# Optimization experiments

Hardware: AMD Instinct MI355X
Metric: run time of the kernel (lower is better)

## Reference

```python
import jax, jax.numpy as jnp
import numpy as np

B, S, IN, E, H, NL = 64, 512, 1024, 128, 8, 4
D = E // H  # head dim = 16


def setup_inputs() -> dict:
    key = jax.random.key(0)
    ks = jax.random.split(key, 12)
    rn = lambda k, shape: jax.random.normal(k, shape, jnp.float32) * 0.02
    x = jax.random.normal(ks[0], (B, S, IN), jnp.float32)
    # per-recording valid lengths; recording 0 full-length so no attention key row is all-masked
    lengths = jax.random.randint(ks[1], (B,), 1, S + 1).at[0].set(S)
    key_padding_mask = jnp.arange(S)[None, :] >= lengths[:, None]  # (B,S) True = pad
    return {
        'x': x,
        'key_padding_mask': key_padding_mask,
        'embed_w': rn(ks[2], (IN, E)), 'embed_b': jnp.zeros((E,), jnp.float32),
        'qkv_w': rn(ks[3], (NL, 3, E, E)), 'qkv_b': jnp.zeros((NL, 3, E), jnp.float32),
        'out_w': rn(ks[4], (NL, E, E)), 'out_b': jnp.zeros((NL, E), jnp.float32),
        'ln_g': jnp.ones((NL, E), jnp.float32), 'ln_b': jnp.zeros((NL, E), jnp.float32),
        'ff1_w': rn(ks[5], (NL, E, 4 * E)), 'ff1_b': jnp.zeros((NL, 4 * E), jnp.float32),
        'ff2_w': rn(ks[6], (NL, 4 * E, E)), 'ff2_b': jnp.zeros((NL, E), jnp.float32),
        'fc1_w': rn(ks[7], (E, 32)), 'fc1_b': jnp.zeros((32,), jnp.float32),
        'fc2_w': rn(ks[8], (32, 1)), 'fc2_b': jnp.zeros((1,), jnp.float32),
    }


def _ln(x, g, b):
    m = x.mean(-1, keepdims=True)
    v = x.var(-1, keepdims=True)
    return (x - m) / jnp.sqrt(v + 1e-5) * g + b


def _pos_enc(s, e):
    pos = jnp.arange(s, dtype=jnp.float32)[:, None]
    i = jnp.arange(e)[None, :]
    angle = pos / jnp.power(jnp.float32(10000.0), (2 * (i // 2)).astype(jnp.float32) / e)
    return jnp.where(i % 2 == 0, jnp.sin(angle), jnp.cos(angle))  # (S,E)


def reference(x, key_padding_mask, embed_w, embed_b, qkv_w, qkv_b, out_w, out_b,
              ln_g, ln_b, ff1_w, ff1_b, ff2_w, ff2_b, fc1_w, fc1_b, fc2_w, fc2_b):
    h = x @ embed_w + embed_b  # (B,S,E)
    pe = _pos_enc(S, E)
    scale = 1.0 / jnp.sqrt(jnp.float32(D))
    # module uses batch_first=False MHA on (B,S,E): attention runs across recordings.
    # key_padding_mask.T -> (S,B): masked keys are recordings, per epoch position.
    keymask = key_padding_mask.T[:, None, None, :]  # (S,1,1,B)
    for l in range(NL):
        h = h + pe[None]  # pos enc re-added every block (as in source)
        res = h
        q = (h @ qkv_w[l, 0] + qkv_b[l, 0]).reshape(B, S, H, D)
        k = (h @ qkv_w[l, 1] + qkv_b[l, 1]).reshape(B, S, H, D)
        v = (h @ qkv_w[l, 2] + qkv_b[l, 2]).reshape(B, S, H, D)
        scores = jnp.einsum('ishd,jshd->shij', q, k) * scale  # (S,H,B,B)
        scores = jnp.where(keymask, -jnp.inf, scores)
        attn = jax.nn.softmax(scores, axis=-1)
        o = jnp.einsum('shij,jshd->ishd', attn, v).reshape(B, S, E)
        o = o @ out_w[l] + out_b[l]
        h = _ln(o + res, ln_g[l], ln_b[l])
        res = h
        ffo = jax.nn.relu(h @ ff1_w[l] + ff1_b[l]) @ ff2_w[l] + ff2_b[l]
        h = _ln(ffo + res, ln_g[l], ln_b[l])  # same LN params reused, as in source
    # masked mean pool over epochs (vectorized replacement of the python loop)
    valid = (~key_padding_mask).astype(h.dtype)  # (B,S)
    mean = jnp.einsum('bse,bs->be', h, valid) / valid.sum(axis=1)[:, None]
    out = jax.nn.relu(mean @ fc1_w + fc1_b) @ fc2_w + fc2_b  # (B,1)
    return jax.nn.sigmoid(out)
```

## Files before the change

kernel.cpp:

```cpp
#include <hip/hip_runtime.h>

#define Bb 64
#define Ss 512
#define INn 1024
#define Ee 128
#define Hh 8
#define Dd 16
#define NLl 4

typedef unsigned short u16;
typedef __attribute__((ext_vector_type(8))) short short8;
typedef __attribute__((ext_vector_type(4))) float f32x4;

__device__ __forceinline__ float b2f(unsigned u) { return __uint_as_float(u << 16); }
__device__ __forceinline__ u16 f2b(float f) {
    unsigned u = __float_as_uint(f);
    unsigned r = u + 0x7FFFu + ((u >> 16) & 1u);
    return (u16)(r >> 16);
}
__device__ __forceinline__ uint2 pk4(float4 f) {
    uint2 r;
    r.x = (unsigned)f2b(f.x) | ((unsigned)f2b(f.y) << 16);
    r.y = (unsigned)f2b(f.z) | ((unsigned)f2b(f.w) << 16);
    return r;
}

#define GLOAD_LDS16(g, l) __builtin_amdgcn_global_load_lds( \
    (const __attribute__((address_space(1))) void*)(g),     \
    (__attribute__((address_space(3))) void*)(l), 16, 0, 0)

#define MFMA16(a, b, c) __builtin_amdgcn_mfma_f32_16x16x32_bf16((a), (b), (c), 0, 0, 0)

__global__ __launch_bounds__(256) void prep_kernel(const unsigned char* __restrict__ m,
                                                   int* __restrict__ lengths,
                                                   float* __restrict__ pe,
                                                   const float* __restrict__ ew,
                                                   const float* __restrict__ qw,
                                                   const float* __restrict__ ow,
                                                   const float* __restrict__ f1w,
                                                   const float* __restrict__ f2w,
                                                   u16* __restrict__ we, u16* __restrict__ wq,
                                                   u16* __restrict__ wo, u16* __restrict__ wf1,
                                                   u16* __restrict__ wf2) {
    const int bid = blockIdx.x, tid = threadIdx.x;
    if (bid == 0) {
        __shared__ int lf[3];
        __shared__ int part[256];
        if (tid < 3) lf[tid] = 0;
        __syncthreads();
        int l0 = 0, l1 = 0, l23 = 0;
        for (int i = tid * 128; i < tid * 128 + 128; ++i) {
            if (m[i]) { int md = i & 3; if (md == 0) l0 = 1; else if (md == 1) l1 = 1; else l23 = 1; }
        }
        if (l0) atomicOr(&lf[0], 1);
        if (l1) atomicOr(&lf[1], 1);
        if (l23) atomicOr(&lf[2], 1);
        __syncthreads();
        int enc = lf[1] ? 1 : (lf[2] ? 2 : 0);
        int b = tid >> 2, q = tid & 3, cnt = 0;
        for (int s = q * 128; s < q * 128 + 128; ++s) {
            int idx = b * Ss + s;
            int mm;
            if (enc == 1)      mm = (m[idx] != 0);
            else if (enc == 2) mm = (((const float*)(const void*)m)[idx] != 0.0f);
            else               mm = (((const int*)(const void*)m)[idx] != 0);
            cnt += (mm == 0);
        }
        part[tid] = cnt;
        __syncthreads();
        if (tid < 64)
            lengths[tid] = part[tid * 4] + part[tid * 4 + 1] + part[tid * 4 + 2] + part[tid * 4 + 3];
        return;
    }
    if (bid <= 32) {
        for (int i = tid; i < 2048; i += 256) {
            int idx = (bid - 1) * 2048 + i;
            int s = idx >> 7, e = idx & 127;
            float expo = (float)(2 * (e >> 1)) * (1.0f / 128.0f);
            float freq = powf(10000.0f, -expo);
            float angle = (float)s * freq;
            pe[idx] = (e & 1) ? cosf(angle) : sinf(angle);
        }
        return;
    }
    int tb = bid - 33;
    const float* src; u16* dst; int K, N, tile;
    if (tb < 32)       { src = ew;  dst = we;  K = 1024; N = 128; tile = tb; }
    else if (tb < 80)  { int b = tb - 32;  int mat = b >> 2; src = qw  + (size_t)mat * 16384; dst = wq  + (size_t)mat * 16384; K = 128; N = 128; tile = b & 3; }
    else if (tb < 96)  { int b = tb - 80;  int mat = b >> 2; src = ow  + (size_t)mat * 16384; dst = wo  + (size_t)mat * 16384; K = 128; N = 128; tile = b & 3; }
    else if (tb < 160) { int b = tb - 96;  int mat = b >> 4; src = f1w + (size_t)mat * 65536; dst = wf1 + (size_t)mat * 65536; K = 128; N = 512; tile = b & 15; }
    else               { int b = tb - 160; int mat = b >> 4; src = f2w + (size_t)mat * 65536; dst = wf2 + (size_t)mat * 65536; K = 512; N = 128; tile = b & 15; }
    int ktiles = K >> 6;
    int k0 = (tile % ktiles) * 64, n0 = (tile / ktiles) * 64;
    __shared__ __align__(16) u16 t_s[64 * 68];
    int r = tid >> 2, cq = (tid & 3) * 16;
    const float* sp = src + (size_t)(k0 + r) * N + n0 + cq;
#pragma unroll
    for (int i = 0; i < 4; ++i) {
        float4 f = *(const float4*)(sp + 4 * i);
        *(uint2*)&t_s[r * 68 + cq + 4 * i] = pk4(f);
    }
    __syncthreads();
    u16 tmp[16];
#pragma unroll
    for (int kk = 0; kk < 16; ++kk) tmp[kk] = t_s[(cq + kk) * 68 + r];
    int rowg = n0 + r;
    int x = (rowg & 7) << 3;
    u16* base = dst + (size_t)rowg * K;
    *(uint4*)(base + ((k0 + cq) ^ x))     = ((uint4*)tmp)[0];
    *(uint4*)(base + ((k0 + cq + 8) ^ x)) = ((uint4*)tmp)[1];
}

__global__ __launch_bounds__(256) void embed_gemm(const float* __restrict__ X,
                                                  const u16* __restrict__ Wt,
                                                  const float* __restrict__ bias,
                                                  const float* __restrict__ pe,
                                                  u16* __restrict__ C) {
    __shared__ __align__(16) u16 Af[64 * 68];
    __shared__ __align__(16) u16 Bs[2][128 * 64];
    const int tid = threadIdx.x;
    const int w = tid >> 6, lane = tid & 63, l16 = lane & 15, lhi = lane >> 4;
    const int row0 = blockIdx.x * 64;
    const int xr = (l16 & 7) << 3;
    f32x4 acc[8];
#pragma unroll
    for (int ni = 0; ni < 8; ++ni) acc[ni] = (f32x4){0.f, 0.f, 0.f, 0.f};

    const int ar = tid >> 2, ak = (tid & 3) * 16;
    const int crow = tid >> 3, cc8 = (tid & 7) * 8;
    const int wave_lds = w * 512;
    const u16* Bbase = Wt + cc8;
    const float* Arow = X + (size_t)(row0 + ar) * 1024 + ak;

#pragma unroll
    for (int i = 0; i < 4; ++i)
        GLOAD_LDS16(Bbase + (size_t)(i * 32 + crow) * 1024, &Bs[0][i * 2048 + wave_lds]);

    for (int it = 0; it < 16; ++it) {
        const int k0 = it * 64;
        __syncthreads();
#pragma unroll
        for (int i = 0; i < 4; ++i) {
            float4 f = *(const float4*)(Arow + k0 + 4 * i);
            *(uint2*)&Af[ar * 68 + ak + 4 * i] = pk4(f);
        }
        __syncthreads();
        if (it < 15) {
#pragma unroll
            for (int i = 0; i < 4; ++i)
                GLOAD_LDS16(Bbase + (size_t)(i * 32 + crow) * 1024 + k0 + 64,
                            &Bs[(it + 1) & 1][i * 2048 + wave_lds]);
        }
#pragma unroll
        for (int ks = 0; ks < 2; ++ks) {
            short8 af;
            ((uint2*)&af)[0] = *(const uint2*)&Af[(w * 16 + l16) * 68 + ks * 32 + lhi * 8];
            ((uint2*)&af)[1] = *(const uint2*)&Af[(w * 16 + l16) * 68 + ks * 32 + lhi * 8 + 4];
#pragma unroll
            for (int ni = 0; ni < 8; ++ni) {
                short8 bfr = *(const short8*)&Bs[it & 1][(ni * 16 + l16) * 64 + ((ks * 32 + lhi * 8) ^ xr)];
                acc[ni] = MFMA16(af, bfr, acc[ni]);
            }
        }
    }
    float biasr[8];
#pragma unroll
    for (int ni = 0; ni < 8; ++ni) biasr[ni] = bias[ni * 16 + l16];
#pragma unroll
    for (int reg = 0; reg < 4; ++reg) {
        int r = row0 + w * 16 + lhi * 4 + reg;
        int s = r & 511;
        int bidx = r >> 9;
        int orow = s * 64 + bidx;
        int xo = (bidx & 7) << 3;
        const float* per = pe + (size_t)s * 128;
        u16* crw = C + (size_t)orow * 128;
#pragma unroll
        for (int ni = 0; ni < 8; ++ni) {
            int c = ni * 16 + l16;
            crw[c ^ xo] = f2b(acc[ni][reg] + biasr[ni] + per[c]);
        }
    }
}

__global__ __launch_bounds__(256) void qkv_gemm(const u16* __restrict__ A,
                                                const u16* __restrict__ Wt,
                                                const float* __restrict__ bias,
                                                u16* __restrict__ Cq,
                                                u16* __restrict__ Ckv) {
    __shared__ __align__(16) u16 As[128 * 128];
    __shared__ __align__(16) u16 Bs[128 * 128];
    const int tid = threadIdx.x, w = tid >> 6, lane = tid & 63;
    const int l16 = lane & 15, lhi = lane >> 4;
    const int row0 = blockIdx.x * 128, col0 = blockIdx.y * 128;
    const int so = w * 512 + lane * 8;
    const int xr = (l16 & 7) << 3;
#pragma unroll
    for (int i = 0; i < 8; ++i) {
        GLOAD_LDS16(A + (size_t)row0 * 128 + i * 2048 + so, &As[i * 2048 + w * 512]);
        GLOAD_LDS16(Wt + (size_t)col0 * 128 + i * 2048 + so, &Bs[i * 2048 + w * 512]);
    }
    __syncthreads();
    f32x4 acc[2][8];
#pragma unroll
    for (int mi = 0; mi < 2; ++mi)
#pragma unroll
        for (int ni = 0; ni < 8; ++ni) acc[mi][ni] = (f32x4){0.f, 0.f, 0.f, 0.f};
#pragma unroll
    for (int ks = 0; ks < 4; ++ks) {
        const int ko = (ks * 32 + lhi * 8) ^ xr;
        short8 af[2], bfr[8];
#pragma unroll
        for (int mi = 0; mi < 2; ++mi)
            af[mi] = *(const short8*)&As[(w * 32 + mi * 16 + l16) * 128 + ko];
#pragma unroll
        for (int ni = 0; ni < 8; ++ni)
            bfr[ni] = *(const short8*)&Bs[(ni * 16 + l16) * 128 + ko];
#pragma unroll
        for (int mi = 0; mi < 2; ++mi)
#pragma unroll
            for (int ni = 0; ni < 8; ++ni)
                acc[mi][ni] = MFMA16(af[mi], bfr[ni], acc[mi][ni]);
    }
    float biasr[8];
#pragma unroll
    for (int ni = 0; ni < 8; ++ni) biasr[ni] = bias[col0 + ni * 16 + l16];
#pragma unroll
    for (int mi = 0; mi < 2; ++mi)
#pragma unroll
        for (int reg = 0; reg < 4; ++reg) {
            int r = row0 + w * 32 + mi * 16 + lhi * 4 + reg;
            u16* crw; int cbase;
            if (col0 == 0) { crw = Cq + (size_t)r * 128; cbase = 0; }
            else           { crw = Ckv + (size_t)r * 256; cbase = col0 - 128; }
#pragma unroll
            for (int ni = 0; ni < 8; ++ni)
                crw[cbase + ni * 16 + l16] = f2b(acc[mi][ni][reg] + biasr[ni]);
        }
}

__global__ __launch_bounds__(256) void attn_ff_kernel(const u16* __restrict__ qb,
                                                      const u16* __restrict__ kvb,
                                                      const u16* __restrict__ wo,
                                                      const float* __restrict__ outb,
                                                      const u16* __restrict__ w1t,
                                                      const u16* __restrict__ w2t,
                                                      const float* __restrict__ b1,
                                                      const float* __restrict__ b2,
                                                      const int* __restrict__ lengths,
                                                      const float* __restrict__ gamma,
                                                      const float* __restrict__ beta,
                                                      const float* __restrict__ pe,
                                                      u16* __restrict__ h) {
    const int d = blockIdx.x;
    const int s = ((d & 7) << 1) + ((d >> 3) & 1) + ((d >> 4) << 4);
    const int tid = threadIdx.x, w = tid >> 6, lane = tid & 63;
    const int l16 = lane & 15, lhi = lane >> 4;
    const int xr = (l16 & 7) << 3;
    const int so = w * 512 + lane * 8;

    __shared__ __align__(16) u16 arena[39424];
    __shared__ int len_s[64];
    u16* o_s  = arena;
    u16* A_s  = arena + 8704;
    u16* T_s  = arena + 16896;
    u16* Ps   = arena + 20992;
    u16* W1_s = arena + 20992;
    u16* W2_s = arena + 29184;

    if (tid < 64) len_s[tid] = lengths[tid];
    __syncthreads();

    bool mk[4];
#pragma unroll
    for (int jt = 0; jt < 4; ++jt) mk[jt] = (s >= len_s[jt * 16 + l16]);

    u16* pw = Ps + w * 4608;
#pragma unroll
    for (int hp = 0; hp < 2; ++hp) {
        const int hh = w * 2 + hp;
        short8 af[4];
#pragma unroll
        for (int it = 0; it < 4; ++it) {
            af[it] = (short8){0, 0, 0, 0, 0, 0, 0, 0};
            if (lhi < 2)
                af[it] = *(const short8*)(qb + ((size_t)(s * 64 + it * 16 + l16)) * 128 + hh * 16 + lhi * 8);
        }
        f32x4 sf[4][4];
#pragma unroll
        for (int jt = 0; jt < 4; ++jt) {
            short8 bf = (short8){0, 0, 0, 0, 0, 0, 0, 0};
            if (lhi < 2)
                bf = *(const short8*)(kvb + ((size_t)(s * 64 + jt * 16 + l16)) * 256 + hh * 16 + lhi * 8);
#pragma unroll
            for (int it = 0; it < 4; ++it) {
                f32x4 z = {0.f, 0.f, 0.f, 0.f};
                sf[it][jt] = MFMA16(af[it], bf, z);
            }
        }
        float inv[4][4];
#pragma unroll
        for (int it = 0; it < 4; ++it) {
#pragma unroll
            for (int reg = 0; reg < 4; ++reg) {
                float vv[4], mx = -1e30f;
#pragma unroll
                for (int jt = 0; jt < 4; ++jt) {
                    float xv = mk[jt] ? -1e30f : sf[it][jt][reg] * 0.25f;
                    vv[jt] = xv; mx = fmaxf(mx, xv);
                }
                mx = fmaxf(mx, __shfl_xor(mx, 1)); mx = fmaxf(mx, __shfl_xor(mx, 2));
                mx = fmaxf(mx, __shfl_xor(mx, 4)); mx = fmaxf(mx, __shfl_xor(mx, 8));
                float e4[4], sum = 0.f;
#pragma unroll
                for (int jt = 0; jt < 4; ++jt) {
                    float e = mk[jt] ? 0.f : __expf(vv[jt] - mx);
                    e4[jt] = e; sum += e;
                }
                sum += __shfl_xor(sum, 1); sum += __shfl_xor(sum, 2);
                sum += __shfl_xor(sum, 4); sum += __shfl_xor(sum, 8);
                inv[it][reg] = 1.0f / sum;
                int prow = it * 16 + lhi * 4 + reg;
#pragma unroll
                for (int jt = 0; jt < 4; ++jt)
                    pw[prow * 72 + jt * 16 + l16] = f2b(e4[jt]);
            }
        }
        f32x4 ao[4];
#pragma unroll
        for (int it = 0; it < 4; ++it) ao[it] = (f32x4){0.f, 0.f, 0.f, 0.f};
        short8 vb[2];
#pragma unroll
        for (int ksv = 0; ksv < 2; ++ksv)
#pragma unroll
            for (int e = 0; e < 8; ++e)
                vb[ksv][e] = (short)kvb[((size_t)(s * 64 + ksv * 32 + lhi * 8 + e)) * 256
                                        + 128 + hh * 16 + l16];
#pragma unroll
        for (int it = 0; it < 4; ++it)
#pragma unroll
            for (int ksv = 0; ksv < 2; ++ksv) {
                short8 pa = *(const short8*)&pw[(it * 16 + l16) * 72 + ksv * 32 + lhi * 8];
                ao[it] = MFMA16(pa, vb[ksv], ao[it]);
            }
#pragma unroll
        for (int it = 0; it < 4; ++it)
#pragma unroll
            for (int reg = 0; reg < 4; ++reg)
                o_s[(it * 16 + lhi * 4 + reg) * 136 + hh * 16 + l16] = f2b(ao[it][reg] * inv[it][reg]);
    }
    __syncthreads();

#pragma unroll
    for (int i = 0; i < 4; ++i) {
        int slot = i * 2048 + so;
        GLOAD_LDS16(w1t + (size_t)(slot >> 7) * 128 + ((slot & 127) ^ (((slot >> 7) & 7) << 3)),
                    &W1_s[slot]);
        GLOAD_LDS16(w2t + (size_t)(slot >> 6) * 512 + ((slot & 63) ^ (((slot >> 6) & 7) << 3)),
                    &W2_s[slot]);
    }

    {
        f32x4 acc[8];
#pragma unroll
        for (int ni = 0; ni < 8; ++ni) acc[ni] = (f32x4){0.f, 0.f, 0.f, 0.f};
#pragma unroll
        for (int ks = 0; ks < 4; ++ks) {
            short8 af = *(const short8*)&o_s[(w * 16 + l16) * 136 + ks * 32 + lhi * 8];
#pragma unroll
            for (int ni = 0; ni < 8; ++ni) {
                short8 bf = *(const short8*)(wo + (size_t)(ni * 16 + l16) * 128 + ((ks * 32 + lhi * 8) ^ xr));
                acc[ni] = MFMA16(af, bf, acc[ni]);
            }
        }
        float biasr[8], gr[8], br[8];
#pragma unroll
        for (int ni = 0; ni < 8; ++ni) {
            int c = ni * 16 + l16;
            biasr[ni] = outb[c]; gr[ni] = gamma[c]; br[ni] = beta[c];
        }
#pragma unroll
        for (int reg = 0; reg < 4; ++reg) {
            int row = w * 16 + lhi * 4 + reg;
            int xo = (row & 7) << 3;
            size_t rbase = ((size_t)(s * 64 + row)) * 128;
            float v[8], sm = 0.f, s2 = 0.f;
#pragma unroll
            for (int ni = 0; ni < 8; ++ni) {
                float x = acc[ni][reg] + biasr[ni] + b2f(h[rbase + ((ni * 16 + l16) ^ xo)]);
                v[ni] = x; sm += x; s2 += x * x;
            }
            sm += __shfl_xor(sm, 1); sm += __shfl_xor(sm, 2);
            sm += __shfl_xor(sm, 4); sm += __shfl_xor(sm, 8);
            s2 += __shfl_xor(s2, 1); s2 += __shfl_xor(s2, 2);
            s2 += __shfl_xor(s2, 4); s2 += __shfl_xor(s2, 8);
            float mean = sm * (1.0f / 128.0f);
            float var = s2 * (1.0f / 128.0f) - mean * mean;
            float rstd = rsqrtf(fmaxf(var, 0.0f) + 1e-5f);
#pragma unroll
            for (int ni = 0; ni < 8; ++ni)
                A_s[row * 128 + ((ni * 16 + l16) ^ xo)] =
                    f2b((v[ni] - mean) * rstd * gr[ni] + br[ni]);
        }
    }
    __syncthreads();

    f32x4 acc2[8];
#pragma unroll
    for (int ni = 0; ni < 8; ++ni) acc2[ni] = (f32x4){0.f, 0.f, 0.f, 0.f};
    for (int nc = 0; nc < 8; ++nc) {
        f32x4 acc1[4];
#pragma unroll
        for (int ni = 0; ni < 4; ++ni) acc1[ni] = (f32x4){0.f, 0.f, 0.f, 0.f};
#pragma unroll
        for (int ks = 0; ks < 4; ++ks) {
            const int ko = (ks * 32 + lhi * 8) ^ xr;
            short8 af = *(const short8*)&A_s[(w * 16 + l16) * 128 + ko];
#pragma unroll
            for (int ni = 0; ni < 4; ++ni) {
                short8 bf = *(const short8*)&W1_s[(ni * 16 + l16) * 128 + ko];
                acc1[ni] = MFMA16(af, bf, acc1[ni]);
            }
        }
        float bb[4];
#pragma unroll
        for (int ni = 0; ni < 4; ++ni) bb[ni] = b1[nc * 64 + ni * 16 + l16];
#pragma unroll
        for (int reg = 0; reg < 4; ++reg) {
            int xt = ((lhi * 4 + reg) & 7) << 3;
#pragma unroll
            for (int ni = 0; ni < 4; ++ni)
                T_s[(w * 16 + lhi * 4 + reg) * 64 + ((ni * 16 + l16) ^ xt)] =
                    f2b(fmaxf(acc1[ni][reg] + bb[ni], 0.0f));
        }
        __syncthreads();
        if (nc < 7) {
#pragma unroll
            for (int i = 0; i < 4; ++i) {
                int slot = i * 2048 + so;
                GLOAD_LDS16(w1t + (size_t)((nc + 1) * 64 + (slot >> 7)) * 128
                                + ((slot & 127) ^ (((slot >> 7) & 7) << 3)),
                            &W1_s[slot]);
            }
        }
#pragma unroll
        for (int ks = 0; ks < 2; ++ks) {
            const int ko = (ks * 32 + lhi * 8) ^ xr;
            short8 pa = *(const short8*)&T_s[(w * 16 + l16) * 64 + ko];
#pragma unroll
            for (int ni = 0; ni < 8; ++ni) {
                short8 bf = *(const short8*)&W2_s[(ni * 16 + l16) * 64 + ko];
                acc2[ni] = MFMA16(pa, bf, acc2[ni]);
            }
        }
        __syncthreads();
        if (nc < 7) {
#pragma unroll
            for (int i = 0; i < 4; ++i) {
                int slot = i * 2048 + so;
                GLOAD_LDS16(w2t + (size_t)(slot >> 6) * 512 + (nc + 1) * 64
                                + ((slot & 63) ^ (((slot >> 6) & 7) << 3)),
                            &W2_s[slot]);
            }
        }
    }
    float b2r[8], gr[8], br[8];
#pragma unroll
    for (int ni = 0; ni < 8; ++ni) {
        int c = ni * 16 + l16;
        b2r[ni] = b2[c]; gr[ni] = gamma[c]; br[ni] = beta[c];
    }
#pragma unroll
    for (int reg = 0; reg < 4; ++reg) {
        int lrow = w * 16 + lhi * 4 + reg;
        int xo = (lrow & 7) << 3;
        float v[8], sm = 0.f, s2 = 0.f;
#pragma unroll
        for (int ni = 0; ni < 8; ++ni) {
            float x = acc2[ni][reg] + b2r[ni] + b2f(A_s[lrow * 128 + ((ni * 16 + l16) ^ xo)]);
            v[ni] = x; sm += x; s2 += x * x;
        }
        sm += __shfl_xor(sm, 1); sm += __shfl_xor(sm, 2);
        sm += __shfl_xor(sm, 4); sm += __shfl_xor(sm, 8);
        s2 += __shfl_xor(s2, 1); s2 += __shfl_xor(s2, 2);
        s2 += __shfl_xor(s2, 4); s2 += __shfl_xor(s2, 8);
        float mean = sm * (1.0f / 128.0f);
        float var = s2 * (1.0f / 128.0f) - mean * mean;
        float rstd = rsqrtf(fmaxf(var, 0.0f) + 1e-5f);
        u16* crw = h + ((size_t)(s * 64 + lrow)) * 128;
#pragma unroll
        for (int ni = 0; ni < 8; ++ni) {
            int c = ni * 16 + l16;
            float val = (v[ni] - mean) * rstd * gr[ni] + br[ni];
            if (pe) val += pe[(size_t)s * 128 + c];
            crw[c ^ xo] = f2b(val);
        }
    }
}

__global__ __launch_bounds__(256) void poolhead_kernel(const u16* __restrict__ h,
                                                       const int* __restrict__ lengths,
                                                       const float* __restrict__ fc1w,
                                                       const float* __restrict__ fc1b,
                                                       const float* __restrict__ fc2w,
                                                       const float* __restrict__ fc2b,
                                                       float* __restrict__ out) {
    int b = blockIdx.x, tid = threadIdx.x;
    int e = tid & 127, half = tid >> 7;
    int len = lengths[b];
    int ep = e ^ ((b & 7) << 3);
    float s = 0.0f;
    for (int t = half; t < len; t += 2) s += b2f(h[((size_t)(t * 64 + b)) * 128 + ep]);
    __shared__ float red[256];
    __shared__ float mp[128];
    __shared__ float z[32];
    red[tid] = s;
    __syncthreads();
    if (tid < 128) mp[tid] = (red[tid] + red[tid + 128]) / (float)len;
    __syncthreads();
    if (tid < 32) {
        float a = fc1b[tid];
        for (int k = 0; k < 128; ++k) a = fmaf(mp[k], fc1w[k * 32 + tid], a);
        z[tid] = fmaxf(a, 0.0f);
    }
    __syncthreads();
    if (tid == 0) {
        float a = fc2b[0];
#pragma unroll
        for (int t = 0; t < 32; ++t) a = fmaf(z[t], fc2w[t], a);
        out[b] = 1.0f / (1.0f + expf(-a));
    }
}

extern "C" void kernel_launch(void* const* d_in, const int* in_sizes, int n_in,
                              void* d_out, int out_size, void* d_ws, size_t ws_size,
                              hipStream_t stream) {
    (void)in_sizes; (void)n_in; (void)out_size; (void)ws_size;
    const float* x        = (const float*)d_in[0];
    const unsigned char* mask = (const unsigned char*)d_in[1];
    const float* embed_w  = (const float*)d_in[2];
    const float* embed_b  = (const float*)d_in[3];
    const float* qkv_w    = (const float*)d_in[4];
    const float* qkv_b    = (const float*)d_in[5];
    const float* out_w    = (const float*)d_in[6];
    const float* out_b    = (const float*)d_in[7];
    const float* ln_g     = (const float*)d_in[8];
    const float* ln_b     = (const float*)d_in[9];
    const float* ff1_w    = (const float*)d_in[10];
    const float* ff1_b    = (const float*)d_in[11];
    const float* ff2_w    = (const float*)d_in[12];
    const float* ff2_b    = (const float*)d_in[13];
    const float* fc1_w    = (const float*)d_in[14];
    const float* fc1_b    = (const float*)d_in[15];
    const float* fc2_w    = (const float*)d_in[16];
    const float* fc2_b    = (const float*)d_in[17];

    char* wsb = (char*)d_ws;
    int*   lengths = (int*)wsb;
    float* pe      = (float*)(wsb + 512);
    u16* wt_embed  = (u16*)(wsb + 262656);
    u16* wt_qkv    = (u16*)(wsb + 524800);
    u16* wt_out    = (u16*)(wsb + 918016);
    u16* wt_ff1    = (u16*)(wsb + 1049088);
    u16* wt_ff2    = (u16*)(wsb + 1573376);
    u16* hbuf      = (u16*)(wsb + 2097664);
    u16* qb        = (u16*)(wsb + 10486272);
    u16* kvb       = (u16*)(wsb + 18874880);

    prep_kernel<<<257, 256, 0, stream>>>(mask, lengths, pe,
                                         embed_w, qkv_w, out_w, ff1_w, ff2_w,
                                         wt_embed, wt_qkv, wt_out, wt_ff1, wt_ff2);

    embed_gemm<<<512, 256, 0, stream>>>(x, wt_embed, embed_b, pe, hbuf);

    for (int l = 0; l < NLl; ++l) {
        qkv_gemm<<<dim3(256, 3), 256, 0, stream>>>(
            hbuf, wt_qkv + (size_t)l * 49152, qkv_b + l * 384, qb, kvb);
        attn_ff_kernel<<<512, 256, 0, stream>>>(
            qb, kvb, wt_out + (size_t)l * 16384, out_b + l * 128,
            wt_ff1 + (size_t)l * 65536, wt_ff2 + (size_t)l * 65536,
            ff1_b + l * 512, ff2_b + l * 128,
            lengths, ln_g + l * 128, ln_b + l * 128,
            (l < 3) ? pe : nullptr, hbuf);
    }

    poolhead_kernel<<<64, 256, 0, stream>>>(hbuf, lengths, fc1_w, fc1_b, fc2_w, fc2_b,
                                            (float*)d_out);
}
```

Before: 376.0 us.

## Fuse next layer's QKV projection into the attention/FFN kernel epilogue

After the final LayerNorm, each attn_ff block keeps its freshly computed hidden tile in shared memory. It then runs the next layer's QKV GEMM in place, double-buffering the weight chunks through the freed W1/W2 shared buffers. Only the first layer's QKV still runs as a separate kernel. This removes three qkv_gemm launches and the global re-read of the hidden state, but lengthens each attn_ff block with extra serialized MFMA work and syncs, and uses only 512 blocks for that GEMM.

Result: slower. 456.7 us (+21.5%).

```diff
diff --git a/kernel.cpp b/kernel.cpp
--- a/kernel.cpp
+++ b/kernel.cpp
@@ -251,7 +251,11 @@
                                                       const float* __restrict__ gamma,
                                                       const float* __restrict__ beta,
                                                       const float* __restrict__ pe,
-                                                      u16* __restrict__ h) {
+                                                      u16* __restrict__ h,
+                                                      const u16* __restrict__ wqn,
+                                                      const float* __restrict__ qbn,
+                                                      u16* __restrict__ qbo,
+                                                      u16* __restrict__ kvbo) {
     const int d = blockIdx.x;
     const int s = ((d & 7) << 1) + ((d >> 3) & 1) + ((d >> 4) << 4);
     const int tid = threadIdx.x, w = tid >> 6, lane = tid & 63;
@@ -464,37 +468,90 @@
             }
         }
     }
-    float b2r[8], gr[8], br[8];
-#pragma unroll
-    for (int ni = 0; ni < 8; ++ni) {
-        int c = ni * 16 + l16;
-        b2r[ni] = b2[c]; gr[ni] = gamma[c]; br[ni] = beta[c];
-    }
-#pragma unroll
-    for (int reg = 0; reg < 4; ++reg) {
-        int lrow = w * 16 + lhi * 4 + reg;
-        int xo = (lrow & 7) << 3;
-        float v[8], sm = 0.f, s2 = 0.f;
-#pragma unroll
-        for (int ni = 0; ni < 8; ++ni) {
-            float x = acc2[ni][reg] + b2r[ni] + b2f(A_s[lrow * 128 + ((ni * 16 + l16) ^ xo)]);
-            v[ni] = x; sm += x; s2 += x * x;
-        }
-        sm += __shfl_xor(sm, 1); sm += __shfl_xor(sm, 2);
-        sm += __shfl_xor(sm, 4); sm += __shfl_xor(sm, 8);
-        s2 += __shfl_xor(s2, 1); s2 += __shfl_xor(s2, 2);
-        s2 += __shfl_xor(s2, 4); s2 += __shfl_xor(s2, 8);
-        float mean = sm * (1.0f / 128.0f);
-        float var = s2 * (1.0f / 128.0f) - mean * mean;
-        float rstd = rsqrtf(fmaxf(var, 0.0f) + 1e-5f);
-        u16* crw = h + ((size_t)(s * 64 + lrow)) * 128;
+    if (wqn) {
+#pragma unroll
+        for (int i = 0; i < 4; ++i) {
+            int slot = i * 2048 + so;
+            GLOAD_LDS16(wqn + slot, &W1_s[slot]);
+        }
+    }
+    {
+        float b2r[8], gr[8], br[8];
 #pragma unroll
         for (int ni = 0; ni < 8; ++ni) {
             int c = ni * 16 + l16;
-            float val = (v[ni] - mean) * rstd * gr[ni] + br[ni];
-            if (pe) val += pe[(size_t)s * 128 + c];
-            crw[c ^ xo] = f2b(val);
-        }
+            b2r[ni] = b2[c]; gr[ni] = gamma[c]; br[ni] = beta[c];
+        }
+#pragma unroll
+        for (int reg = 0; reg < 4; ++reg) {
+            int lrow = w * 16 + lhi * 4 + reg;
+            int xo = (lrow & 7) << 3;
+            float v[8], sm = 0.f, s2 = 0.f;
+#pragma unroll
+            for (int ni = 0; ni < 8; ++ni) {
+                float x = acc2[ni][reg] + b2r[ni] + b2f(A_s[lrow * 128 + ((ni * 16 + l16) ^ xo)]);
+                v[ni] = x; sm += x; s2 += x * x;
+            }
+            sm += __shfl_xor(sm, 1); sm += __shfl_xor(sm, 2);
+            sm += __shfl_xor(sm, 4); sm += __shfl_xor(sm, 8);
+            s2 += __shfl_xor(s2, 1); s2 += __shfl_xor(s2, 2);
+            s2 += __shfl_xor(s2, 4); s2 += __shfl_xor(s2, 8);
+            float mean = sm * (1.0f / 128.0f);
+            float var = s2 * (1.0f / 128.0f) - mean * mean;
+            float rstd = rsqrtf(fmaxf(var, 0.0f) + 1e-5f);
+            u16* crw = h + ((size_t)(s * 64 + lrow)) * 128;
+#pragma unroll
+            for (int ni = 0; ni < 8; ++ni) {
+                int c = ni * 16 + l16;
+                float val = (v[ni] - mean) * rstd * gr[ni] + br[ni];
+                if (pe) val += pe[(size_t)s * 128 + c];
+                u16 hv = f2b(val);
+                crw[c ^ xo] = hv;
+                if (wqn) A_s[lrow * 128 + (c ^ xo)] = hv;
+            }
+        }
+    }
+    if (!wqn) return;
+
+    __syncthreads();
+    for (int c = 0; c < 6; ++c) {
+        u16* Wcur = (c & 1) ? W2_s : W1_s;
+        u16* Wnxt = (c & 1) ? W1_s : W2_s;
+        if (c < 5) {
+#pragma unroll
+            for (int i = 0; i < 4; ++i) {
+                int slot = i * 2048 + so;
+                GLOAD_LDS16(wqn + (c + 1) * 8192 + slot, &Wnxt[slot]);
+            }
+        }
+        f32x4 acc[4];
+#pragma unroll
+        for (int ni = 0; ni < 4; ++ni) acc[ni] = (f32x4){0.f, 0.f, 0.f, 0.f};
+#pragma unroll
+        for (int ks = 0; ks < 4; ++ks) {
+            const int ko = (ks * 32 + lhi * 8) ^ xr;
+            short8 af = *(const short8*)&A_s[(w * 16 + l16) * 128 + ko];
+#pragma unroll
+            for (int ni = 0; ni < 4; ++ni) {
+                short8 bf = *(const short8*)&Wcur[(ni * 16 + l16) * 128 + ko];
+                acc[ni] = MFMA16(af, bf, acc[ni]);
+            }
+        }
+        float bb[4];
+#pragma unroll
+        for (int ni = 0; ni < 4; ++ni) bb[ni] = qbn[c * 64 + ni * 16 + l16];
+#pragma unroll
+        for (int reg = 0; reg < 4; ++reg) {
+            int row = w * 16 + lhi * 4 + reg;
+#pragma unroll
+            for (int ni = 0; ni < 4; ++ni) {
+                int col = c * 64 + ni * 16 + l16;
+                u16 v = f2b(acc[ni][reg] + bb[ni]);
+                if (c < 2) qbo[((size_t)(s * 64 + row)) * 128 + col] = v;
+                else       kvbo[((size_t)(s * 64 + row)) * 256 + col - 128] = v;
+            }
+        }
+        __syncthreads();
     }
 }
 
@@ -573,15 +630,19 @@
 
     embed_gemm<<<512, 256, 0, stream>>>(x, wt_embed, embed_b, pe, hbuf);
 
+    qkv_gemm<<<dim3(256, 3), 256, 0, stream>>>(hbuf, wt_qkv, qkv_b, qb, kvb);
+
     for (int l = 0; l < NLl; ++l) {
-        qkv_gemm<<<dim3(256, 3), 256, 0, stream>>>(
-            hbuf, wt_qkv + (size_t)l * 49152, qkv_b + l * 384, qb, kvb);
+        bool mq = (l < 3);
         attn_ff_kernel<<<512, 256, 0, stream>>>(
             qb, kvb, wt_out + (size_t)l * 16384, out_b + l * 128,
             wt_ff1 + (size_t)l * 65536, wt_ff2 + (size_t)l * 65536,
             ff1_b + l * 512, ff2_b + l * 128,
             lengths, ln_g + l * 128, ln_b + l * 128,
-            (l < 3) ? pe : nullptr, hbuf);
+            (l < 3) ? pe : nullptr, hbuf,
+            mq ? wt_qkv + (size_t)(l + 1) * 49152 : nullptr,
+            mq ? qkv_b + (l + 1) * 384 : nullptr,
+            qb, kvb);
     }
 
     poolhead_kernel<<<64, 256, 0, stream>>>(hbuf, lengths, fc1_w, fc1_b, fc2_w, fc2_b,
```
